# Kernel optimization log

Hardware: AMD Instinct MI355X
Metric: run time of the kernel (lower is better)

## Reference

```python
import jax, jax.numpy as jnp
import numpy as np

H = 12          # num heads
D = 768         # hidden size
DH = D // H     # size per head
FF = 3072       # intermediate size
EPS = 1e-11


def gelu(x):
    # tanh approximation, matching the TF source exactly
    c = np.sqrt(2.0 / np.pi).astype(np.float32)
    return x * 0.5 * (1.0 + jnp.tanh(c * (x + 0.044715 * jnp.power(x, 3))))


def layer_norm(x, gamma, beta):
    mean = jnp.mean(x, axis=-1, keepdims=True)
    var = jnp.mean(jnp.square(x - mean), axis=-1, keepdims=True)
    return (x - mean) * jax.lax.rsqrt(var + EPS) * gamma + beta


def setup_inputs() -> dict:
    key = jax.random.key(0)
    ks = jax.random.split(key, 12)
    B, S = 16, 512
    std = 0.02
    inp = {
        "x": jax.random.normal(ks[0], (B, S, D), jnp.float32),
        "mask": jnp.ones((B, S), dtype=bool),
        "Wq": jax.random.normal(ks[1], (D, D), jnp.float32) * std,
        "bq": jnp.zeros((D,), jnp.float32),
        "Wk": jax.random.normal(ks[2], (D, D), jnp.float32) * std,
        "bk": jnp.zeros((D,), jnp.float32),
        "Wv": jax.random.normal(ks[3], (D, D), jnp.float32) * std,
        "bv": jnp.zeros((D,), jnp.float32),
        "Wo": jax.random.normal(ks[4], (D, D), jnp.float32) * std,
        "bo": jnp.zeros((D,), jnp.float32),
        "g1": jnp.ones((D,), jnp.float32),
        "b1": jnp.zeros((D,), jnp.float32),
        "Wi": jax.random.normal(ks[5], (D, FF), jnp.float32) * std,
        "bi": jnp.zeros((FF,), jnp.float32),
        "Wo2": jax.random.normal(ks[6], (FF, D), jnp.float32) * std,
        "bo2": jnp.zeros((D,), jnp.float32),
        "g2": jnp.ones((D,), jnp.float32),
        "b2": jnp.zeros((D,), jnp.float32),
    }
    return inp


def reference(x, mask, Wq, bq, Wk, bk, Wv, bv, Wo, bo, g1, b1, Wi, bi, Wo2, bo2, g2, b2):
    B, S, _ = x.shape
    # QKV projections
    q = (x @ Wq + bq).reshape(B, S, H, DH)
    k = (x @ Wk + bk).reshape(B, S, H, DH)
    v = (x @ Wv + bv).reshape(B, S, H, DH)
    # scaled dot-product attention scores [B, H, S, S]
    scores = jnp.einsum("bqhd,bkhd->bhqk", q, k) / np.sqrt(DH).astype(np.float32)
    # key-side mask, applied as score * m + (1 - m) * -100 (per original source)
    m = mask[:, None, None, :].astype(jnp.float32)
    scores = scores * m + (1.0 - m) * (-100.0)
    probs = jax.nn.softmax(scores, axis=-1)
    attn = jnp.einsum("bhqk,bkhd->bqhd", probs, v).reshape(B, S, D)
    # tf.boolean_mask with all-True mask -> flatten batch and seq dims
    attn = attn.reshape(B * S, D)
    x_flat = x.reshape(B * S, D)
    # attention output projection + residual + LN
    attn_out = layer_norm(attn @ Wo + bo + x_flat, g1, b1)
    # FFN: gelu dense then output dense + residual + LN
    inter = gelu(attn_out @ Wi + bi)
    out = layer_norm(inter @ Wo2 + bo2 + attn_out, g2, b2)
    return out
```

## Files before the change

### kernel.cpp

```cpp
#include <hip/hip_runtime.h>


#define DEV __device__ __forceinline__

typedef unsigned short u16;
typedef unsigned int   u32;
typedef __bf16 bf16x8 __attribute__((ext_vector_type(8)));
typedef float  f32x4  __attribute__((ext_vector_type(4)));
typedef unsigned short u16x8 __attribute__((ext_vector_type(8)));
typedef unsigned short u16x4 __attribute__((ext_vector_type(4)));

DEV u16 f2bf(float f) {
    u32 u = __builtin_bit_cast(u32, f);
    u += 0x7fffu + ((u >> 16) & 1u);
    return (u16)(u >> 16);
}
DEV float bf2f(u16 u) { u32 x = (u32)u << 16; return __builtin_bit_cast(float, x); }

DEV float gelu_f(float x) {
    float u = 0.7978845608028654f * (x + 0.044715f * x * x * x);
    float e = __expf(2.f * u);
    return 0.5f * x * (2.f - 2.f / (e + 1.f));
}

DEV void gload16(const void* gsrc, void* ldst) {
    __builtin_amdgcn_global_load_lds(
        (__attribute__((address_space(1))) void*)(void*)(const_cast<void*>(gsrc)),
        (__attribute__((address_space(3))) void*)ldst, 16, 0, 0);
}

DEV f32x4 MFMA(bf16x8 a, bf16x8 b, f32x4 c) {
    return __builtin_amdgcn_mfma_f32_16x16x32_bf16(a, b, c, 0, 0, 0);
}

__global__ __launch_bounds__(256) void prep(
    const float* __restrict__ x, const float* __restrict__ Wq,
    const float* __restrict__ Wk, const float* __restrict__ Wv,
    const float* __restrict__ Wo, const float* __restrict__ Wi,
    const float* __restrict__ Wo2, const float* __restrict__ bq,
    const float* __restrict__ bk, const float* __restrict__ bv,
    u16* __restrict__ Xb, u16* __restrict__ WqkvT, u16* __restrict__ WoT,
    u16* __restrict__ WiT, u16* __restrict__ Wo2T, float* __restrict__ bqkv) {
    __shared__ float tile[32][33];
    int bid = blockIdx.x, t = threadIdx.x;
    if (bid < 6144) {
        int i = (bid * 256 + t) * 4;
        f32x4 v = *(const f32x4*)(x + i);
        u16x4 o;
        o.x = f2bf(v.x); o.y = f2bf(v.y); o.z = f2bf(v.z); o.w = f2bf(v.w);
        *(u16x4*)(Xb + i) = o;
        return;
    }
    bid -= 6144;
    if (bid >= 6912) {
        int i = (bid - 6912) * 256 + t;
        if (i < 2304)
            bqkv[i] = (i < 768) ? bq[i] : (i < 1536 ? bk[i - 768] : bv[i - 1536]);
        return;
    }
    const float* in; u16* out; int R, C, bx, by;
    if (bid < 1728) {
        int w = bid / 576, idx = bid % 576;
        in = (w == 0) ? Wq : (w == 1) ? Wk : Wv;
        out = WqkvT + (size_t)w * 768 * 768;
        R = 768; C = 768; bx = idx % 24; by = idx / 24;
    } else if (bid < 2304) {
        int idx = bid - 1728;
        in = Wo; out = WoT; R = 768; C = 768; bx = idx % 24; by = idx / 24;
    } else if (bid < 4608) {
        int idx = bid - 2304;
        in = Wi; out = WiT; R = 768; C = 3072; bx = idx % 96; by = idx / 96;
    } else {
        int idx = bid - 4608;
        in = Wo2; out = Wo2T; R = 3072; C = 768; bx = idx % 24; by = idx / 24;
    }
    int tx = t & 31, ty = t >> 5;
    int r0 = by * 32, c0 = bx * 32;
#pragma unroll
    for (int i = 0; i < 4; i++)
        tile[ty + i * 8][tx] = in[(size_t)(r0 + ty + i * 8) * C + c0 + tx];
    __syncthreads();
#pragma unroll
    for (int i = 0; i < 4; i++)
        out[(size_t)(c0 + ty + i * 8) * R + r0 + tx] = f2bf(tile[tx][ty + i * 8]);
}

template <int EPI>
DEV void gemm_c3_body(const u16* __restrict__ A, const u16* __restrict__ BT,
                      const float* __restrict__ bias, const void* __restrict__ res,
                      void* __restrict__ Cout, int N, int K, int ntn) {
    __shared__ __align__(16) char smem[49152];
    const int t = threadIdx.x, lane = t & 63, wid = t >> 6;
    const int nwg = gridDim.x, bid = blockIdx.x;
    const int swzb = ((nwg & 7) == 0) ? ((bid & 7) * (nwg >> 3) + (bid >> 3)) : bid;
    const int tm = swzb / ntn, tn = swzb % ntn;
    const int wm = wid >> 1, wn = wid & 1;

    f32x4 acc[4][4];
#pragma unroll
    for (int i = 0; i < 4; i++)
#pragma unroll
        for (int j = 0; j < 4; j++) acc[i][j] = f32x4{0.f, 0.f, 0.f, 0.f};

    const int NT = K >> 5;
    const u16* Ab = A + (size_t)tm * 128 * K;
    const u16* Bb = BT + (size_t)tn * 128 * K;

    int sr[2], sc[2];
#pragma unroll
    for (int j = 0; j < 2; j++) {
        int X = t * 16 + j * 4096;
        int Y = X ^ (((X >> 7) & 7) << 4);
        sr[j] = Y >> 6; sc[j] = (Y & 63) >> 1;
    }
    const u16* pA0 = Ab + (size_t)sr[0] * K + sc[0];
    const u16* pA1 = Ab + (size_t)sr[1] * K + sc[1];
    const u16* pB0 = Bb + (size_t)sr[0] * K + sc[0];
    const u16* pB1 = Bb + (size_t)sr[1] * K + sc[1];
    const int d0 = wid * 1024, d1 = wid * 1024 + 4096;

    const int g16 = (lane >> 4) << 4;
    const int rA = wm * 64 + (lane & 15);
    const int rB = wn * 64 + (lane & 15);
    const int aoff = (rA * 64 + g16) ^ (((rA >> 1) & 7) << 4);
    const int boff = 8192 + ((rB * 64 + g16) ^ (((rB >> 1) & 7) << 4));

#define STG(TT)                                                       \
    {                                                                 \
        char* s_ = smem + ((TT) % 3) * 16384;                         \
        int ko_ = (TT) * 32;                                          \
        gload16(pA0 + ko_, s_ + d0);                                  \
        gload16(pA1 + ko_, s_ + d1);                                  \
        gload16(pB0 + ko_, s_ + 8192 + d0);                           \
        gload16(pB1 + ko_, s_ + 8192 + d1);                           \
    }

    STG(0) STG(1)
    asm volatile("s_waitcnt vmcnt(4)" ::: "memory");
    __builtin_amdgcn_s_barrier();
    asm volatile("" ::: "memory");

    for (int tt = 0; tt < NT; ++tt) {
        if (tt + 2 < NT) STG(tt + 2)
        const char* buf = smem + (tt % 3) * 16384;
        bf16x8 af[4], bfr[4];
#pragma unroll
        for (int mi = 0; mi < 4; mi++) af[mi] = *(const bf16x8*)(buf + aoff + mi * 1024);
#pragma unroll
        for (int ni = 0; ni < 4; ni++) bfr[ni] = *(const bf16x8*)(buf + boff + ni * 1024);
        __builtin_amdgcn_s_setprio(1);
#pragma unroll
        for (int mi = 0; mi < 4; mi++)
#pragma unroll
            for (int ni = 0; ni < 4; ni++)
                acc[mi][ni] = MFMA(af[mi], bfr[ni], acc[mi][ni]);
        __builtin_amdgcn_s_setprio(0);
        if (tt + 1 < NT) {
            if (tt + 2 < NT) asm volatile("s_waitcnt vmcnt(4)" ::: "memory");
            else             asm volatile("s_waitcnt vmcnt(0)" ::: "memory");
        }
        __builtin_amdgcn_s_barrier();
        asm volatile("" ::: "memory");
    }
#undef STG

    const int r0 = tm * 128 + wm * 64, c0 = tn * 128 + wn * 64;
    float bcol[4];
#pragma unroll
    for (int ni = 0; ni < 4; ni++) bcol[ni] = bias[c0 + ni * 16 + (lane & 15)];
#pragma unroll
    for (int mi = 0; mi < 4; mi++) {
#pragma unroll
        for (int r = 0; r < 4; r++) {
            int gr = r0 + mi * 16 + ((lane >> 4) << 2) + r;
#pragma unroll
            for (int ni = 0; ni < 4; ni++) {
                int gc = c0 + ni * 16 + (lane & 15);
                float v = acc[mi][ni][r] + bcol[ni];
                if constexpr (EPI == 2) v = gelu_f(v);
                if constexpr (EPI == 3)
                    v += ((const float*)res)[(size_t)gr * N + gc];
                if constexpr (EPI == 4)
                    v += bf2f(((const u16*)res)[(size_t)gr * N + gc]);
                ((u16*)Cout)[(size_t)gr * N + gc] = f2bf(v);
            }
        }
    }
}

__global__ __launch_bounds__(256, 3) void g3_qkv(const u16* A, const u16* BT,
                                                 const float* bias, void* C,
                                                 int N, int K, int ntn) {
    gemm_c3_body<0>(A, BT, bias, nullptr, C, N, K, ntn);
}
__global__ __launch_bounds__(256, 3) void g3_ffn1(const u16* A, const u16* BT,
                                                  const float* bias, void* C,
                                                  int N, int K, int ntn) {
    gemm_c3_body<2>(A, BT, bias, nullptr, C, N, K, ntn);
}
__global__ __launch_bounds__(256, 3) void g3_wo(const u16* A, const u16* BT,
                                                const float* bias, const void* res,
                                                void* C, int N, int K, int ntn) {
    gemm_c3_body<3>(A, BT, bias, res, C, N, K, ntn);
}
__global__ __launch_bounds__(256, 3) void g3_ffn2(const u16* A, const u16* BT,
                                                  const float* bias, const void* res,
                                                  void* C, int N, int K, int ntn) {
    gemm_c3_body<4>(A, BT, bias, res, C, N, K, ntn);
}

__global__ __launch_bounds__(256) void attn_kernel(const u16* __restrict__ QKV,
                                                   u16* __restrict__ attnb) {
    __shared__ __align__(16) char sm[24576];
    char* Ks = sm;
    char* Vt = sm + 8192;
    const int t = threadIdx.x, lane = t & 63, wid = t >> 6;
    const int qt = blockIdx.x, bh = blockIdx.y;
    const int b = bh / 12, h = bh % 12;
    const size_t base = (size_t)b * 512 * 2304;
    char* Pw = sm + 16384 + wid * 2048;

    bf16x8 aq[2];
    {
        int qrow = qt * 64 + wid * 16 + (lane & 15);
        const u16* qp = QKV + base + (size_t)qrow * 2304 + h * 64 + ((lane >> 4) << 3);
        aq[0] = *(const bf16x8*)qp;
        aq[1] = *(const bf16x8*)(qp + 32);
    }
    f32x4 oacc[4];
#pragma unroll
    for (int g = 0; g < 4; g++) oacc[g] = f32x4{0.f, 0.f, 0.f, 0.f};
    float mrun[4] = {-1e30f, -1e30f, -1e30f, -1e30f};
    float lrun[4] = {0.f, 0.f, 0.f, 0.f};

    for (int kt = 0; kt < 8; ++kt) {
        __syncthreads();
#pragma unroll
        for (int i = 0; i < 2; i++) {
            int cw = wid * 2 + i;
            int o = cw * 1024 + lane * 16;
            int row = o >> 7;
            int cb = (o & 127) ^ ((row & 7) << 4);
            gload16(QKV + base + (size_t)(kt * 64 + row) * 2304 + 768 + h * 64 + (cb >> 1),
                    Ks + cw * 1024);
        }
        {
            int key = t & 63, dh0 = wid * 16;
            const u16* vp = QKV + base + (size_t)(kt * 64 + key) * 2304 + 1536 + h * 64 + dh0;
            u16x8 v0 = *(const u16x8*)vp;
            u16x8 v1 = *(const u16x8*)(vp + 8);
#pragma unroll
            for (int j = 0; j < 8; j++) {
                int dh = dh0 + j;
                *(u16*)(Vt + dh * 128 + ((key * 2) ^ ((dh & 7) << 4))) = v0[j];
            }
#pragma unroll
            for (int j = 0; j < 8; j++) {
                int dh = dh0 + 8 + j;
                *(u16*)(Vt + dh * 128 + ((key * 2) ^ ((dh & 7) << 4))) = v1[j];
            }
        }
        __syncthreads();

        f32x4 sacc[4];
#pragma unroll
        for (int ni = 0; ni < 4; ni++) sacc[ni] = f32x4{0.f, 0.f, 0.f, 0.f};
#pragma unroll
        for (int ni = 0; ni < 4; ni++) {
            int row = ni * 16 + (lane & 15);
#pragma unroll
            for (int ks = 0; ks < 2; ks++) {
                int cb = (ks * 64 + ((lane >> 4) << 4)) ^ ((row & 7) << 4);
                bf16x8 bk = *(const bf16x8*)(Ks + row * 128 + cb);
                sacc[ni] = MFMA(aq[ks], bk, sacc[ni]);
            }
        }
#pragma unroll
        for (int ni = 0; ni < 4; ni++)
#pragma unroll
            for (int r = 0; r < 4; r++) sacc[ni][r] *= 0.125f;

#pragma unroll
        for (int r = 0; r < 4; r++) {
            float pm = fmaxf(fmaxf(sacc[0][r], sacc[1][r]), fmaxf(sacc[2][r], sacc[3][r]));
            pm = fmaxf(pm, __shfl_xor(pm, 1));
            pm = fmaxf(pm, __shfl_xor(pm, 2));
            pm = fmaxf(pm, __shfl_xor(pm, 4));
            pm = fmaxf(pm, __shfl_xor(pm, 8));
            float mnew = fmaxf(mrun[r], pm);
            float sf = __expf(mrun[r] - mnew);
            mrun[r] = mnew;
            lrun[r] *= sf;
#pragma unroll
            for (int g = 0; g < 4; g++) oacc[g][r] *= sf;
            int prow = ((lane >> 4) << 2) + r;
            float ps = 0.f;
#pragma unroll
            for (int ni = 0; ni < 4; ni++) {
                float p = __expf(sacc[ni][r] - mnew);
                ps += p;
                int col = ni * 16 + (lane & 15);
                *(u16*)(Pw + prow * 128 + ((col * 2) ^ ((prow & 7) << 4))) = f2bf(p);
            }
            ps += __shfl_xor(ps, 1);
            ps += __shfl_xor(ps, 2);
            ps += __shfl_xor(ps, 4);
            ps += __shfl_xor(ps, 8);
            lrun[r] += ps;
        }
        __syncthreads();

#pragma unroll
        for (int ks = 0; ks < 2; ks++) {
            int prow = lane & 15;
            int pcb = (ks * 64 + ((lane >> 4) << 4)) ^ ((prow & 7) << 4);
            bf16x8 ap = *(const bf16x8*)(Pw + prow * 128 + pcb);
#pragma unroll
            for (int g = 0; g < 4; g++) {
                int vrow = g * 16 + (lane & 15);
                int vcb = (ks * 64 + ((lane >> 4) << 4)) ^ ((vrow & 7) << 4);
                bf16x8 bv = *(const bf16x8*)(Vt + vrow * 128 + vcb);
                oacc[g] = MFMA(ap, bv, oacc[g]);
            }
        }
    }

#pragma unroll
    for (int g = 0; g < 4; g++)
#pragma unroll
        for (int r = 0; r < 4; r++) {
            int qrow = qt * 64 + wid * 16 + ((lane >> 4) << 2) + r;
            float o = oacc[g][r] / lrun[r];
            attnb[(size_t)(b * 512 + qrow) * 768 + h * 64 + g * 16 + (lane & 15)] = f2bf(o);
        }
}

template <int OUTF>
__global__ __launch_bounds__(256) void ln_s(const u16* __restrict__ S,
                                            const float* __restrict__ g,
                                            const float* __restrict__ bta,
                                            void* __restrict__ out) {
    int row = blockIdx.x, t = threadIdx.x, lane = t & 63, wid = t >> 6;
    const u16* s = S + (size_t)row * 768;
    float v[3];
#pragma unroll
    for (int i = 0; i < 3; i++) v[i] = bf2f(s[t + i * 256]);

    float sum = v[0] + v[1] + v[2];
#pragma unroll
    for (int o = 32; o; o >>= 1) sum += __shfl_xor(sum, o);
    __shared__ float sm[4];
    __shared__ float bc[2];
    if (lane == 0) sm[wid] = sum;
    __syncthreads();
    if (t == 0) bc[0] = (sm[0] + sm[1] + sm[2] + sm[3]) * (1.f / 768.f);
    __syncthreads();
    float mean = bc[0];

    float q = 0.f;
#pragma unroll
    for (int i = 0; i < 3; i++) { float d = v[i] - mean; q += d * d; }
#pragma unroll
    for (int o = 32; o; o >>= 1) q += __shfl_xor(q, o);
    if (lane == 0) sm[wid] = q;
    __syncthreads();
    if (t == 0) bc[1] = rsqrtf((sm[0] + sm[1] + sm[2] + sm[3]) * (1.f / 768.f) + 1e-11f);
    __syncthreads();
    float rs = bc[1];
#pragma unroll
    for (int i = 0; i < 3; i++) {
        int c = t + i * 256;
        float o = (v[i] - mean) * rs * g[c] + bta[c];
        if constexpr (OUTF)
            ((float*)out)[(size_t)row * 768 + c] = o;
        else
            ((u16*)out)[(size_t)row * 768 + c] = f2bf(o);
    }
}

extern "C" void kernel_launch(void* const* d_in, const int* in_sizes, int n_in,
                              void* d_out, int out_size, void* d_ws, size_t ws_size,
                              hipStream_t stream) {
    const float* x   = (const float*)d_in[0];
    const float* Wq  = (const float*)d_in[2];
    const float* bq  = (const float*)d_in[3];
    const float* Wk  = (const float*)d_in[4];
    const float* bk  = (const float*)d_in[5];
    const float* Wv  = (const float*)d_in[6];
    const float* bv  = (const float*)d_in[7];
    const float* Wo  = (const float*)d_in[8];
    const float* bo  = (const float*)d_in[9];
    const float* g1  = (const float*)d_in[10];
    const float* b1  = (const float*)d_in[11];
    const float* Wi  = (const float*)d_in[12];
    const float* bi  = (const float*)d_in[13];
    const float* Wo2 = (const float*)d_in[14];
    const float* bo2 = (const float*)d_in[15];
    const float* g2  = (const float*)d_in[16];
    const float* b2  = (const float*)d_in[17];

    char* w = (char*)d_ws;
    size_t off = 0;
    auto alloc = [&](size_t n) { size_t o = off; off += (n + 255) & ~(size_t)255; return o; };
    size_t oXb    = alloc((size_t)8192 * 768 * 2);
    size_t oWqkvT = alloc((size_t)2304 * 768 * 2);
    size_t oWoT   = alloc((size_t)768 * 768 * 2);
    size_t oWiT   = alloc((size_t)3072 * 768 * 2);
    size_t oWo2T  = alloc((size_t)768 * 3072 * 2);
    size_t oBqkv  = alloc((size_t)2304 * 4);
    size_t oR0    = alloc((size_t)8192 * 3072 * 2);
    size_t oYb    = alloc((size_t)8192 * 768 * 2);
    size_t oAob   = alloc((size_t)8192 * 768 * 2);
    (void)ws_size; (void)in_sizes; (void)n_in; (void)out_size;

    u16*   Xb    = (u16*)(w + oXb);
    u16*   WqkvT = (u16*)(w + oWqkvT);
    u16*   WoT   = (u16*)(w + oWoT);
    u16*   WiT   = (u16*)(w + oWiT);
    u16*   Wo2T  = (u16*)(w + oWo2T);
    float* bqkv  = (float*)(w + oBqkv);
    u16*   QKV   = (u16*)(w + oR0);
    u16*   attnb = (u16*)(w + oR0 + (size_t)8192 * 2304 * 2);
    u16*   inter = (u16*)(w + oR0);
    u16*   Yb    = (u16*)(w + oYb);
    u16*   aob   = (u16*)(w + oAob);

    prep<<<13065, 256, 0, stream>>>(x, Wq, Wk, Wv, Wo, Wi, Wo2, bq, bk, bv,
                                    Xb, WqkvT, WoT, WiT, Wo2T, bqkv);
    g3_qkv<<<1152, 256, 0, stream>>>(Xb, WqkvT, bqkv, QKV, 2304, 768, 18);
    attn_kernel<<<dim3(8, 192), 256, 0, stream>>>(QKV, attnb);
    g3_wo<<<384, 256, 0, stream>>>(attnb, WoT, bo, x, Yb, 768, 768, 6);
    ln_s<0><<<8192, 256, 0, stream>>>(Yb, g1, b1, aob);
    g3_ffn1<<<1536, 256, 0, stream>>>(aob, WiT, bi, inter, 3072, 768, 24);
    g3_ffn2<<<384, 256, 0, stream>>>(inter, Wo2T, bo2, aob, Yb, 768, 3072, 6);
    ln_s<1><<<8192, 256, 0, stream>>>(Yb, g2, b2, (float*)d_out);
}
```

Before: 261.6 us.

## Double-buffer K/V tiles in attention kernel to overlap loads with compute

The attention kernel now uses two shared-memory buffers for the K and V tiles. The next tile's global loads are issued before the current tile's QK^T, softmax and PV work, and the transposed V stores and barrier are deferred to the end of each iteration. This hides global-memory latency and removes one barrier per iteration. The cost is a larger shared-memory footprint (40 KB instead of 24 KB), which may reduce occupancy. It also drops the barrier between the per-wave P writes and reads, which relies on each wave only reading its own P region.

```diff
diff --git a/kernel.cpp b/kernel.cpp
--- a/kernel.cpp
+++ b/kernel.cpp
@@ -211,14 +211,20 @@
 
 __global__ __launch_bounds__(256) void attn_kernel(const u16* __restrict__ QKV,
                                                    u16* __restrict__ attnb) {
-    __shared__ __align__(16) char sm[24576];
-    char* Ks = sm;
-    char* Vt = sm + 8192;
+    __shared__ __align__(16) char sm[40960];
     const int t = threadIdx.x, lane = t & 63, wid = t >> 6;
     const int qt = blockIdx.x, bh = blockIdx.y;
     const int b = bh / 12, h = bh % 12;
     const size_t base = (size_t)b * 512 * 2304;
-    char* Pw = sm + 16384 + wid * 2048;
+    char* Pw = sm + 32768 + wid * 2048;
+
+    const int scw = wid * 2;
+    const int so0 = scw * 1024 + lane * 16;
+    const int so1 = so0 + 1024;
+    const int srow0 = so0 >> 7, srow1 = so1 >> 7;
+    const int scb0 = (so0 & 127) ^ ((srow0 & 7) << 4);
+    const int scb1 = (so1 & 127) ^ ((srow1 & 7) << 4);
+    const int vkey = t & 63, vdh0 = wid * 16;
 
     bf16x8 aq[2];
     {
@@ -233,34 +239,41 @@
     float mrun[4] = {-1e30f, -1e30f, -1e30f, -1e30f};
     float lrun[4] = {0.f, 0.f, 0.f, 0.f};
 
+    gload16(QKV + base + (size_t)srow0 * 2304 + 768 + h * 64 + (scb0 >> 1), sm + scw * 1024);
+    gload16(QKV + base + (size_t)srow1 * 2304 + 768 + h * 64 + (scb1 >> 1), sm + scw * 1024 + 1024);
+    {
+        const u16* vp = QKV + base + (size_t)vkey * 2304 + 1536 + h * 64 + vdh0;
+        u16x8 v0 = *(const u16x8*)vp;
+        u16x8 v1 = *(const u16x8*)(vp + 8);
+        char* Vt = sm + 8192;
+#pragma unroll
+        for (int j = 0; j < 8; j++) {
+            int dh = vdh0 + j;
+            *(u16*)(Vt + dh * 128 + ((vkey * 2) ^ ((dh & 7) << 4))) = v0[j];
+        }
+#pragma unroll
+        for (int j = 0; j < 8; j++) {
+            int dh = vdh0 + 8 + j;
+            *(u16*)(Vt + dh * 128 + ((vkey * 2) ^ ((dh & 7) << 4))) = v1[j];
+        }
+    }
+    asm volatile("s_waitcnt vmcnt(0)" ::: "memory");
+    __syncthreads();
+
     for (int kt = 0; kt < 8; ++kt) {
-        __syncthreads();
-#pragma unroll
-        for (int i = 0; i < 2; i++) {
-            int cw = wid * 2 + i;
-            int o = cw * 1024 + lane * 16;
-            int row = o >> 7;
-            int cb = (o & 127) ^ ((row & 7) << 4);
-            gload16(QKV + base + (size_t)(kt * 64 + row) * 2304 + 768 + h * 64 + (cb >> 1),
-                    Ks + cw * 1024);
-        }
-        {
-            int key = t & 63, dh0 = wid * 16;
-            const u16* vp = QKV + base + (size_t)(kt * 64 + key) * 2304 + 1536 + h * 64 + dh0;
-            u16x8 v0 = *(const u16x8*)vp;
-            u16x8 v1 = *(const u16x8*)(vp + 8);
-#pragma unroll
-            for (int j = 0; j < 8; j++) {
-                int dh = dh0 + j;
-                *(u16*)(Vt + dh * 128 + ((key * 2) ^ ((dh & 7) << 4))) = v0[j];
-            }
-#pragma unroll
-            for (int j = 0; j < 8; j++) {
-                int dh = dh0 + 8 + j;
-                *(u16*)(Vt + dh * 128 + ((key * 2) ^ ((dh & 7) << 4))) = v1[j];
-            }
-        }
-        __syncthreads();
+        const int d = kt & 1;
+        const char* Ks = sm + d * 16384;
+        const char* Vt = sm + d * 16384 + 8192;
+        u16x8 nv0, nv1;
+        if (kt < 7) {
+            char* Kn = sm + (d ^ 1) * 16384;
+            const size_t krow = (size_t)((kt + 1) * 64);
+            gload16(QKV + base + (krow + srow0) * 2304 + 768 + h * 64 + (scb0 >> 1), Kn);
+            gload16(QKV + base + (krow + srow1) * 2304 + 768 + h * 64 + (scb1 >> 1), Kn + 1024);
+            const u16* vp = QKV + base + (krow + vkey) * 2304 + 1536 + h * 64 + vdh0;
+            nv0 = *(const u16x8*)vp;
+            nv1 = *(const u16x8*)(vp + 8);
+        }
 
         f32x4 sacc[4];
 #pragma unroll
@@ -308,7 +321,6 @@
             ps += __shfl_xor(ps, 8);
             lrun[r] += ps;
         }
-        __syncthreads();
 
 #pragma unroll
         for (int ks = 0; ks < 2; ks++) {
@@ -323,6 +335,22 @@
                 oacc[g] = MFMA(ap, bv, oacc[g]);
             }
         }
+
+        if (kt < 7) {
+            char* Vn = sm + (d ^ 1) * 16384 + 8192;
+#pragma unroll
+            for (int j = 0; j < 8; j++) {
+                int dh = vdh0 + j;
+                *(u16*)(Vn + dh * 128 + ((vkey * 2) ^ ((dh & 7) << 4))) = nv0[j];
+            }
+#pragma unroll
+            for (int j = 0; j < 8; j++) {
+                int dh = vdh0 + 8 + j;
+                *(u16*)(Vn + dh * 128 + ((vkey * 2) ^ ((dh & 7) << 4))) = nv1[j];
+            }
+        }
+        asm volatile("s_waitcnt vmcnt(0)" ::: "memory");
+        __syncthreads();
     }
 
 #pragma unroll
```

Result: no change. 256.4 us (-2.0%).
